# Kernel tuning notes

Hardware: AMD Instinct MI355X
Metric: run time of the kernel (lower is better)

The kernel has to match this reference:

```python
import jax, jax.numpy as jnp
import numpy as np

DIM = 512
QK_DIM = 128
HIDDEN = 1024


def setup_inputs() -> dict:
    key = jax.random.key(0)
    ks = jax.random.split(key, 8)
    b, n = 4, 4096
    x = jax.random.normal(ks[0], (b, n, DIM), dtype=jnp.float32)
    # nn.Linear(dim, hidden*2)
    w_hidden = jax.random.normal(ks[1], (DIM, 2 * HIDDEN), dtype=jnp.float32) / np.sqrt(DIM)
    b_hidden = jnp.zeros((2 * HIDDEN,), dtype=jnp.float32)
    # nn.Linear(dim, qk_dim, bias=False)
    w_qk = jax.random.normal(ks[2], (DIM, QK_DIM), dtype=jnp.float32) / np.sqrt(DIM)
    # OffsetScale params (gamma init 1, beta init 0; randomize slightly for a nontrivial test)
    q_gamma = 1.0 + 0.02 * jax.random.normal(ks[3], (QK_DIM,), dtype=jnp.float32)
    q_beta = 0.02 * jax.random.normal(ks[4], (QK_DIM,), dtype=jnp.float32)
    k_gamma = 1.0 + 0.02 * jax.random.normal(ks[5], (QK_DIM,), dtype=jnp.float32)
    k_beta = 0.02 * jax.random.normal(ks[6], (QK_DIM,), dtype=jnp.float32)
    # nn.Linear(hidden, dim)
    w_out = jax.random.normal(ks[7], (HIDDEN, DIM), dtype=jnp.float32) / np.sqrt(HIDDEN)
    b_out = jnp.zeros((DIM,), dtype=jnp.float32)
    return {
        "x": x,
        "w_hidden": w_hidden, "b_hidden": b_hidden,
        "w_qk": w_qk,
        "q_gamma": q_gamma, "q_beta": q_beta,
        "k_gamma": k_gamma, "k_beta": k_beta,
        "w_out": w_out, "b_out": b_out,
    }


def reference(x, w_hidden, b_hidden, w_qk, q_gamma, q_beta, k_gamma, k_beta, w_out, b_out):
    scale = QK_DIM ** -0.5
    # to_hidden -> chunk into v, gate (NOTE: source applies no activation here)
    hid = jnp.einsum('bnd,dh->bnh', x, w_hidden) + b_hidden  # [b, n, 2*hidden]
    v, gate = jnp.split(hid, 2, axis=-1)                     # each [b, n, hidden]
    qk = jnp.einsum('bnd,de->bne', x, w_qk)                  # [b, n, qk_dim]
    q = qk * q_gamma + q_beta
    k = qk * k_gamma + k_beta
    sim = jnp.einsum('bid,bjd->bij', q, k) * scale           # [b, n, n]
    attn = jnp.square(jax.nn.relu(sim))                      # ReLU^2, no softmax
    out = jnp.einsum('bij,bjh->bih', attn, v)                # [b, n, hidden]
    out = out * gate
    out = jnp.einsum('bnh,hd->bnd', out, w_out) + b_out      # [b, n, dim]
    return out + x  # add_residual=True
```

## Files before the change

### kernel.cpp

```cpp
#include <hip/hip_runtime.h>
#include <hip/hip_bf16.h>

typedef __attribute__((ext_vector_type(8))) short bf16x8;
typedef __attribute__((ext_vector_type(4))) float f32x4;
typedef unsigned short u16;

__device__ __forceinline__ u16 f2b(float f) {
  __hip_bfloat16 h = __float2bfloat16(f);
  return __builtin_bit_cast(unsigned short, h);
}
__device__ __forceinline__ float b2f(u16 u) {
  __hip_bfloat16 h = __builtin_bit_cast(__hip_bfloat16, u);
  return __bfloat162float(h);
}

#define BAR() __builtin_amdgcn_s_barrier()
#define LGKM0() do { asm volatile("s_waitcnt lgkmcnt(0)" ::: "memory"); __builtin_amdgcn_sched_barrier(0); } while (0)
#define LGKM4() do { asm volatile("s_waitcnt lgkmcnt(4)" ::: "memory"); __builtin_amdgcn_sched_barrier(0); } while (0)
#define LGKM8() do { asm volatile("s_waitcnt lgkmcnt(8)" ::: "memory"); __builtin_amdgcn_sched_barrier(0); } while (0)
#define VMCNT4() asm volatile("s_waitcnt vmcnt(4)" ::: "memory")
#define VMCNT0() asm volatile("s_waitcnt vmcnt(0)" ::: "memory")

#define EPI_HID 0
#define EPI_QK 1
#define EPI_ATTN 2
#define EPI_PV 3
#define EPI_OUT 4

__device__ __forceinline__ void stage_tile(char* sbase, const char* gbase, int ld_bytes, int tid) {
#pragma unroll
  for (int i = 0; i < 4; ++i) {
    int o = (i * 256 + tid) * 16;
    int row = o >> 7;
    int cb = o & 127;
    int scb = cb ^ ((row & 7) << 4);
    const char* src = gbase + (long)row * ld_bytes + scb;
    __builtin_amdgcn_global_load_lds((const __attribute__((address_space(1))) void*)src,
                                     (__attribute__((address_space(3))) void*)(sbase + o),
                                     16, 0, 0);
  }
}

template <int EPI>
__global__ __launch_bounds__(256, 2) void gemm_tn(
    const char* Ab, const char* Bb, long sAbat, long sBbat,
    int lda_b, int ldb_b, int nkt,
    u16* o0, u16* o1,
    const float* a0, const float* a1, const float* a2, const float* a3,
    float* fout, const float* xres) {
  __shared__ __align__(16) char lds[32768];
  char* sA = lds;
  char* sB = lds + 16384;
  const int tid = threadIdx.x;
  const int lane = tid & 63;
  const int wave = tid >> 6;
  const int wm = wave >> 1, wn = wave & 1;
  const int l16 = lane & 15, lq = lane >> 4;
  const int bat = blockIdx.z;
  const int row0 = blockIdx.y * 128;
  const int col0 = blockIdx.x * 128;

  const char* Abase = Ab + (long)bat * sAbat + (long)row0 * lda_b;
  const char* Bbase = Bb + (long)bat * sBbat + (long)col0 * ldb_b;

  f32x4 acc[4][4];
#pragma unroll
  for (int i = 0; i < 4; ++i)
#pragma unroll
    for (int j = 0; j < 4; ++j) acc[i][j] = (f32x4){0.f, 0.f, 0.f, 0.f};

  for (int kt = 0; kt < nkt; ++kt) {
    stage_tile(sA, Abase + (long)kt * 128, lda_b, tid);
    stage_tile(sB, Bbase + (long)kt * 128, ldb_b, tid);
    __syncthreads();
#pragma unroll
    for (int kk = 0; kk < 2; ++kk) {
      bf16x8 af[4], bfr[4];
#pragma unroll
      for (int mf = 0; mf < 4; ++mf) {
        int r = wm * 64 + mf * 16 + l16;
        int kb = kk * 64 + lq * 16;
        af[mf] = *(const bf16x8*)(sA + r * 128 + (kb ^ ((r & 7) << 4)));
      }
#pragma unroll
      for (int nf = 0; nf < 4; ++nf) {
        int r = wn * 64 + nf * 16 + l16;
        int kb = kk * 64 + lq * 16;
        bfr[nf] = *(const bf16x8*)(sB + r * 128 + (kb ^ ((r & 7) << 4)));
      }
#pragma unroll
      for (int mf = 0; mf < 4; ++mf)
#pragma unroll
        for (int nf = 0; nf < 4; ++nf)
          acc[mf][nf] = __builtin_amdgcn_mfma_f32_16x16x32_bf16(af[mf], bfr[nf], acc[mf][nf], 0, 0, 0);
    }
    __syncthreads();
  }

#pragma unroll
  for (int mf = 0; mf < 4; ++mf) {
#pragma unroll
    for (int nf = 0; nf < 4; ++nf) {
      const int row = row0 + wm * 64 + mf * 16 + lq * 4;
      const int col = col0 + wn * 64 + nf * 16 + l16;
      f32x4 v = acc[mf][nf];
      if constexpr (EPI == EPI_QK) {
        float qg = a0[col], qbt = a1[col], kg = a2[col], kbt = a3[col];
#pragma unroll
        for (int i = 0; i < 4; ++i) {
          float t = v[i];
          o0[(size_t)(row + i) * 128 + col] = f2b(t * qg + qbt);
          o1[(size_t)(row + i) * 128 + col] = f2b(t * kg + kbt);
        }
      } else if constexpr (EPI == EPI_OUT) {
        float bias = a0[col];
#pragma unroll
        for (int i = 0; i < 4; ++i)
          fout[(size_t)(row + i) * 512 + col] = v[i] + bias + xres[(size_t)(row + i) * 512 + col];
      }
    }
  }
}

__device__ __forceinline__ void stage_half(char* sbase, const char* gbase, long ld, int tid) {
#pragma unroll
  for (int i = 0; i < 2; ++i) {
    int o = (i * 512 + tid) * 16;
    int row = o >> 7;
    int cb = o & 127;
    int scb = cb ^ ((row & 7) << 4);
    const char* src = gbase + (long)row * ld + scb;
    __builtin_amdgcn_global_load_lds((const __attribute__((address_space(1))) void*)src,
                                     (__attribute__((address_space(3))) void*)(sbase + o),
                                     16, 0, 0);
  }
}

template <int EPI>
__global__ __launch_bounds__(512, 2) void gemm256(
    const char* Ab, const char* Bb, long sAbat, long sBbat,
    long lda, long ldb, int nkt, int nx,
    u16* o0, u16* o1,
    const float* a0, float* fout, const float* xres) {
  extern __shared__ __align__(16) char lds[];
  const int tid = threadIdx.x;
  const int lane = tid & 63;
  const int wave = tid >> 6;
  const int wm = wave >> 2;
  const int wn = wave & 3;
  const int l16 = lane & 15, lq = lane >> 4;
  const int bat = blockIdx.y;

  const int nwg = gridDim.x;
  const int qq = nwg >> 3;
  const int fid = blockIdx.x;
  const int swz = (fid & 7) * qq + (fid >> 3);
  const int row0 = (swz / nx) * 256;
  const int col0 = (swz % nx) * 256;

  const char* gA = Ab + (long)bat * sAbat + (long)row0 * lda;
  const char* gB = Bb + (long)bat * sBbat + (long)col0 * ldb;

  f32x4 acc[8][4];
#pragma unroll
  for (int i = 0; i < 8; ++i)
#pragma unroll
    for (int j = 0; j < 4; ++j) acc[i][j] = (f32x4){0.f, 0.f, 0.f, 0.f};

  const int kmask = (l16 & 7) << 4;
  const int kb0 = (lq * 16) ^ kmask;
  const int kb1 = (64 + lq * 16) ^ kmask;

  stage_half(lds + 32768, gB, ldb, tid);
  stage_half(lds + 32768 + 16384, gB + 128 * ldb, ldb, tid);
  stage_half(lds, gA, lda, tid);
  stage_half(lds + 16384, gA + 128 * lda, lda, tid);
  if (nkt > 1) {
    stage_half(lds + 65536 + 32768, gB + 128, ldb, tid);
    stage_half(lds + 65536 + 32768 + 16384, gB + 128 * ldb + 128, ldb, tid);
    VMCNT4();
  } else {
    VMCNT0();
  }
  BAR();

  bf16x8 af0[4], af1[4], afp0[4], afp1[4], bfr0[4], bfr1[4];

  for (int t = 0; t < nkt; ++t) {
    const char* buf = lds + (t & 1) * 65536;
    const char* myA = buf + wm * 16384;
    const char* myB = buf + 32768 + (wn >> 1) * 16384;
    const int rB = (wn & 1) * 64;
    char* stA = lds + ((t + 1) & 1) * 65536;
    char* stB = lds + (t & 1) * 65536 + 32768;
    const bool sA_ok = (t + 1) < nkt;
    const bool sB_ok = (t + 2) < nkt;

#pragma unroll
    for (int nf = 0; nf < 4; ++nf)
      bfr0[nf] = *(const bf16x8*)(myB + (rB + nf * 16 + l16) * 128 + kb0);
#pragma unroll
    for (int mf = 0; mf < 4; ++mf)
      af0[mf] = *(const bf16x8*)(myA + (mf * 16 + l16) * 128 + kb0);
#pragma unroll
    for (int nf = 0; nf < 4; ++nf)
      bfr1[nf] = *(const bf16x8*)(myB + (rB + nf * 16 + l16) * 128 + kb1);
#pragma unroll
    for (int mf = 0; mf < 4; ++mf)
      af1[mf] = *(const bf16x8*)(myA + (mf * 16 + l16) * 128 + kb1);
    if (sA_ok) stage_half(stA, gA + (long)(t + 1) * 128, lda, tid);
    BAR();
    LGKM8();
    __builtin_amdgcn_s_setprio(1);
#pragma unroll
    for (int mf = 0; mf < 4; ++mf)
#pragma unroll
      for (int nf = 0; nf < 4; ++nf)
        acc[mf][nf] = __builtin_amdgcn_mfma_f32_16x16x32_bf16(af0[mf], bfr0[nf], acc[mf][nf], 0, 0, 0);
    __builtin_amdgcn_s_setprio(0);
    BAR();

#pragma unroll
    for (int mf = 0; mf < 4; ++mf)
      afp0[mf] = *(const bf16x8*)(myA + (64 + mf * 16 + l16) * 128 + kb0);
    if (sA_ok) stage_half(stA + 16384, gA + 128 * lda + (long)(t + 1) * 128, lda, tid);
    BAR();
    LGKM4();
    __builtin_amdgcn_s_setprio(1);
#pragma unroll
    for (int mf = 0; mf < 4; ++mf)
#pragma unroll
      for (int nf = 0; nf < 4; ++nf)
        acc[mf][nf] = __builtin_amdgcn_mfma_f32_16x16x32_bf16(af1[mf], bfr1[nf], acc[mf][nf], 0, 0, 0);
    __builtin_amdgcn_s_setprio(0);
    BAR();

#pragma unroll
    for (int mf = 0; mf < 4; ++mf)
      afp1[mf] = *(const bf16x8*)(myA + (64 + mf * 16 + l16) * 128 + kb1);
    if (sB_ok) stage_half(stB, gB + (long)(t + 2) * 128, ldb, tid);
    BAR();
    LGKM4();
    __builtin_amdgcn_s_setprio(1);
#pragma unroll
    for (int mf = 0; mf < 4; ++mf)
#pragma unroll
      for (int nf = 0; nf < 4; ++nf)
        acc[4 + mf][nf] = __builtin_amdgcn_mfma_f32_16x16x32_bf16(afp0[mf], bfr0[nf], acc[4 + mf][nf], 0, 0, 0);
    __builtin_amdgcn_s_setprio(0);
    BAR();

    if (sB_ok) stage_half(stB + 16384, gB + 128 * ldb + (long)(t + 2) * 128, ldb, tid);
    BAR();
    LGKM0();
    __builtin_amdgcn_s_setprio(1);
#pragma unroll
    for (int mf = 0; mf < 4; ++mf)
#pragma unroll
      for (int nf = 0; nf < 4; ++nf)
        acc[4 + mf][nf] = __builtin_amdgcn_mfma_f32_16x16x32_bf16(afp1[mf], bfr1[nf], acc[4 + mf][nf], 0, 0, 0);
    __builtin_amdgcn_s_setprio(0);
    if (sB_ok) { VMCNT4(); } else if (sA_ok) { VMCNT0(); }
    BAR();
  }

#pragma unroll
  for (int mi = 0; mi < 8; ++mi) {
#pragma unroll
    for (int ni = 0; ni < 4; ++ni) {
      const int row = row0 + wm * 128 + mi * 16 + lq * 4;
      const int col = col0 + wn * 64 + ni * 16 + l16;
      f32x4 v = acc[mi][ni];
      if constexpr (EPI == EPI_HID) {
        float bias = a0[col];
        u16* dst = (col < 1024) ? (o0 + (size_t)col * 16384 + row)
                                : (o1 + (size_t)(col - 1024) * 16384 + row);
        *(ushort4*)dst = make_ushort4(f2b(v.x + bias), f2b(v.y + bias), f2b(v.z + bias), f2b(v.w + bias));
      } else if constexpr (EPI == EPI_ATTN) {
        const float scale = 0.088388347648318447f;
        u16* dst = o0 + (size_t)bat * 4096 * 4096;
#pragma unroll
        for (int i = 0; i < 4; ++i) {
          float t = v[i] * scale;
          t = t > 0.f ? t * t : 0.f;
          dst[(size_t)(row + i) * 4096 + col] = f2b(t);
        }
      } else if constexpr (EPI == EPI_PV) {
        const u16* gt = o1 + (size_t)col * 16384 + (size_t)bat * 4096 + row;
        ushort4 g = *(const ushort4*)gt;
        u16* dst = o0 + (size_t)bat * 4096 * 1024;
        dst[(size_t)(row + 0) * 1024 + col] = f2b(v.x * b2f(g.x));
        dst[(size_t)(row + 1) * 1024 + col] = f2b(v.y * b2f(g.y));
        dst[(size_t)(row + 2) * 1024 + col] = f2b(v.z * b2f(g.z));
        dst[(size_t)(row + 3) * 1024 + col] = f2b(v.w * b2f(g.w));
      }
    }
  }
}

__global__ void conv_b(const float* in, u16* out, int n) {
  int i = (blockIdx.x * blockDim.x + threadIdx.x) * 4;
  if (i >= n) return;
  float4 f = *(const float4*)(in + i);
  *(ushort4*)(out + i) = make_ushort4(f2b(f.x), f2b(f.y), f2b(f.z), f2b(f.w));
}

__global__ void transpose_b(const float* in, u16* out, int R, int C) {
  int o = blockIdx.x * blockDim.x + threadIdx.x;
  if (o >= R * C) return;
  int c = o / R, r = o - c * R;
  out[o] = f2b(in[(size_t)r * C + c]);
}

extern "C" void kernel_launch(void* const* d_in, const int* in_sizes, int n_in,
                              void* d_out, int out_size, void* d_ws, size_t ws_size,
                              hipStream_t stream) {
  const float* x = (const float*)d_in[0];
  const float* w_hidden = (const float*)d_in[1];
  const float* b_hidden = (const float*)d_in[2];
  const float* w_qk = (const float*)d_in[3];
  const float* q_gamma = (const float*)d_in[4];
  const float* q_beta = (const float*)d_in[5];
  const float* k_gamma = (const float*)d_in[6];
  const float* k_beta = (const float*)d_in[7];
  const float* w_out = (const float*)d_in[8];
  const float* b_out = (const float*)d_in[9];
  float* out = (float*)d_out;

  char* ws = (char*)d_ws;
  size_t off = 0;
  auto alloc = [&](size_t bytes) { char* p = ws + off; off += (bytes + 255) & ~255ull; return p; };
  u16* xb     = (u16*)alloc(16384ull * 512 * 2);
  u16* wh_t   = (u16*)alloc(2048ull * 512 * 2);
  u16* wqk_t  = (u16*)alloc(128ull * 512 * 2);
  u16* wout_t = (u16*)alloc(512ull * 1024 * 2);
  u16* v_t    = (u16*)alloc(1024ull * 16384 * 2);
  u16* g_t    = (u16*)alloc(1024ull * 16384 * 2);
  u16* qb_a   = (u16*)alloc(16384ull * 128 * 2);
  u16* kb_a   = (u16*)alloc(16384ull * 128 * 2);
  u16* attnb  = (u16*)alloc(4ull * 4096 * 4096 * 2);
  u16* out1b  = (u16*)alloc(16384ull * 1024 * 2);

  (void)hipFuncSetAttribute((const void*)gemm256<EPI_HID>, hipFuncAttributeMaxDynamicSharedMemorySize, 131072);
  (void)hipFuncSetAttribute((const void*)gemm256<EPI_ATTN>, hipFuncAttributeMaxDynamicSharedMemorySize, 131072);
  (void)hipFuncSetAttribute((const void*)gemm256<EPI_PV>, hipFuncAttributeMaxDynamicSharedMemorySize, 131072);

  conv_b<<<(16384 * 512 / 4 + 255) / 256, 256, 0, stream>>>(x, xb, 16384 * 512);
  transpose_b<<<(512 * 2048 + 255) / 256, 256, 0, stream>>>(w_hidden, wh_t, 512, 2048);
  transpose_b<<<(512 * 128 + 255) / 256, 256, 0, stream>>>(w_qk, wqk_t, 512, 128);
  transpose_b<<<(1024 * 512 + 255) / 256, 256, 0, stream>>>(w_out, wout_t, 1024, 512);

  gemm256<EPI_HID><<<dim3(512, 1), 512, 131072, stream>>>(
      (const char*)xb, (const char*)wh_t, 0, 0, 1024, 1024, 8, 8,
      v_t, g_t, b_hidden, nullptr, nullptr);
  gemm_tn<EPI_QK><<<dim3(1, 128, 1), 256, 0, stream>>>(
      (const char*)xb, (const char*)wqk_t, 0, 0, 1024, 1024, 8,
      qb_a, kb_a, q_gamma, q_beta, k_gamma, k_beta, nullptr, nullptr);
  gemm256<EPI_ATTN><<<dim3(256, 4), 512, 131072, stream>>>(
      (const char*)qb_a, (const char*)kb_a, 4096ll * 256, 4096ll * 256, 256, 256, 2, 16,
      attnb, nullptr, nullptr, nullptr, nullptr);
  gemm256<EPI_PV><<<dim3(64, 4), 512, 131072, stream>>>(
      (const char*)attnb, (const char*)v_t, 4096ll * 8192, 8192, 8192, 32768, 64, 4,
      out1b, g_t, nullptr, nullptr, nullptr);
  gemm_tn<EPI_OUT><<<dim3(4, 128, 1), 256, 0, stream>>>(
      (const char*)out1b, (const char*)wout_t, 0, 0, 2048, 2048, 16,
      nullptr, nullptr, b_out, nullptr, nullptr, nullptr, out, x);
}
```

Before: 322.8 us.

## Software-pipeline LDS fragment loads across k-tiles and route output GEMM through gemm256

The main 256x256 GEMM loop now prefetches the first-half A/B fragments for the next k-tile during the last MFMA phase. It also drops most of the per-phase workgroup barriers, keeping only one vmcnt-gated barrier before the next-tile reads plus one at loop end. Separately, the final output projection moves from the smaller gemm_tn kernel to gemm256 with the residual/bias epilogue, launched as 128 workgroups. Fewer barriers means less synchronisation stall, but removing them risks LDS races where staging overwrites buffers other waves may still be reading. The 128-block output launch may also underfill the GPU.

```diff
diff --git a/kernel.cpp b/kernel.cpp
--- a/kernel.cpp
+++ b/kernel.cpp
@@ -19,6 +19,7 @@
 #define LGKM4() do { asm volatile("s_waitcnt lgkmcnt(4)" ::: "memory"); __builtin_amdgcn_sched_barrier(0); } while (0)
 #define LGKM8() do { asm volatile("s_waitcnt lgkmcnt(8)" ::: "memory"); __builtin_amdgcn_sched_barrier(0); } while (0)
 #define VMCNT4() asm volatile("s_waitcnt vmcnt(4)" ::: "memory")
+#define VMCNT2() asm volatile("s_waitcnt vmcnt(2)" ::: "memory")
 #define VMCNT0() asm volatile("s_waitcnt vmcnt(0)" ::: "memory")
 
 #define EPI_HID 0
@@ -112,11 +113,6 @@
           o0[(size_t)(row + i) * 128 + col] = f2b(t * qg + qbt);
           o1[(size_t)(row + i) * 128 + col] = f2b(t * kg + kbt);
         }
-      } else if constexpr (EPI == EPI_OUT) {
-        float bias = a0[col];
-#pragma unroll
-        for (int i = 0; i < 4; ++i)
-          fout[(size_t)(row + i) * 512 + col] = v[i] + bias + xres[(size_t)(row + i) * 512 + col];
       }
     }
   }
@@ -170,6 +166,7 @@
   const int kmask = (l16 & 7) << 4;
   const int kb0 = (lq * 16) ^ kmask;
   const int kb1 = (64 + lq * 16) ^ kmask;
+  const int rB = (wn & 1) * 64;
 
   stage_half(lds + 32768, gB, ldb, tid);
   stage_half(lds + 32768 + 16384, gB + 128 * ldb, ldb, tid);
@@ -185,31 +182,36 @@
   BAR();
 
   bf16x8 af0[4], af1[4], afp0[4], afp1[4], bfr0[4], bfr1[4];
+  {
+    const char* myA = lds + wm * 16384;
+    const char* myB = lds + 32768 + (wn >> 1) * 16384;
+#pragma unroll
+    for (int nf = 0; nf < 4; ++nf)
+      bfr0[nf] = *(const bf16x8*)(myB + (rB + nf * 16 + l16) * 128 + kb0);
+#pragma unroll
+    for (int mf = 0; mf < 4; ++mf)
+      af0[mf] = *(const bf16x8*)(myA + (mf * 16 + l16) * 128 + kb0);
+  }
 
   for (int t = 0; t < nkt; ++t) {
-    const char* buf = lds + (t & 1) * 65536;
-    const char* myA = buf + wm * 16384;
-    const char* myB = buf + 32768 + (wn >> 1) * 16384;
-    const int rB = (wn & 1) * 64;
-    char* stA = lds + ((t + 1) & 1) * 65536;
-    char* stB = lds + (t & 1) * 65536 + 32768;
+    const char* bufc = lds + (t & 1) * 65536;
+    const char* bufn = lds + ((t + 1) & 1) * 65536;
+    const char* myA = bufc + wm * 16384;
+    const char* myB = bufc + 32768 + (wn >> 1) * 16384;
+    const char* nA = bufn + wm * 16384;
+    const char* nB = bufn + 32768 + (wn >> 1) * 16384;
+    char* stA = (char*)bufn;
+    char* stB = (char*)bufc + 32768;
     const bool sA_ok = (t + 1) < nkt;
     const bool sB_ok = (t + 2) < nkt;
 
 #pragma unroll
     for (int nf = 0; nf < 4; ++nf)
-      bfr0[nf] = *(const bf16x8*)(myB + (rB + nf * 16 + l16) * 128 + kb0);
-#pragma unroll
-    for (int mf = 0; mf < 4; ++mf)
-      af0[mf] = *(const bf16x8*)(myA + (mf * 16 + l16) * 128 + kb0);
-#pragma unroll
-    for (int nf = 0; nf < 4; ++nf)
       bfr1[nf] = *(const bf16x8*)(myB + (rB + nf * 16 + l16) * 128 + kb1);
 #pragma unroll
     for (int mf = 0; mf < 4; ++mf)
       af1[mf] = *(const bf16x8*)(myA + (mf * 16 + l16) * 128 + kb1);
     if (sA_ok) stage_half(stA, gA + (long)(t + 1) * 128, lda, tid);
-    BAR();
     LGKM8();
     __builtin_amdgcn_s_setprio(1);
 #pragma unroll
@@ -218,13 +220,11 @@
       for (int nf = 0; nf < 4; ++nf)
         acc[mf][nf] = __builtin_amdgcn_mfma_f32_16x16x32_bf16(af0[mf], bfr0[nf], acc[mf][nf], 0, 0, 0);
     __builtin_amdgcn_s_setprio(0);
-    BAR();
 
 #pragma unroll
     for (int mf = 0; mf < 4; ++mf)
       afp0[mf] = *(const bf16x8*)(myA + (64 + mf * 16 + l16) * 128 + kb0);
     if (sA_ok) stage_half(stA + 16384, gA + 128 * lda + (long)(t + 1) * 128, lda, tid);
-    BAR();
     LGKM4();
     __builtin_amdgcn_s_setprio(1);
 #pragma unroll
@@ -239,7 +239,6 @@
     for (int mf = 0; mf < 4; ++mf)
       afp1[mf] = *(const bf16x8*)(myA + (64 + mf * 16 + l16) * 128 + kb1);
     if (sB_ok) stage_half(stB, gB + (long)(t + 2) * 128, ldb, tid);
-    BAR();
     LGKM4();
     __builtin_amdgcn_s_setprio(1);
 #pragma unroll
@@ -248,11 +247,21 @@
       for (int nf = 0; nf < 4; ++nf)
         acc[4 + mf][nf] = __builtin_amdgcn_mfma_f32_16x16x32_bf16(afp0[mf], bfr0[nf], acc[4 + mf][nf], 0, 0, 0);
     __builtin_amdgcn_s_setprio(0);
-    BAR();
-
+    if (sA_ok) {
+      if (sB_ok) { VMCNT2(); } else { VMCNT0(); }
+      BAR();
+    }
+
+    if (sA_ok) {
+#pragma unroll
+      for (int nf = 0; nf < 4; ++nf)
+        bfr0[nf] = *(const bf16x8*)(nB + (rB + nf * 16 + l16) * 128 + kb0);
+#pragma unroll
+      for (int mf = 0; mf < 4; ++mf)
+        af0[mf] = *(const bf16x8*)(nA + (mf * 16 + l16) * 128 + kb0);
+    }
     if (sB_ok) stage_half(stB + 16384, gB + 128 * ldb + (long)(t + 2) * 128, ldb, tid);
-    BAR();
-    LGKM0();
+    if (sA_ok) { LGKM8(); } else { LGKM0(); }
     __builtin_amdgcn_s_setprio(1);
 #pragma unroll
     for (int mf = 0; mf < 4; ++mf)
@@ -260,7 +269,6 @@
       for (int nf = 0; nf < 4; ++nf)
         acc[4 + mf][nf] = __builtin_amdgcn_mfma_f32_16x16x32_bf16(afp1[mf], bfr1[nf], acc[4 + mf][nf], 0, 0, 0);
     __builtin_amdgcn_s_setprio(0);
-    if (sB_ok) { VMCNT4(); } else if (sA_ok) { VMCNT0(); }
     BAR();
   }
 
@@ -293,6 +301,11 @@
         dst[(size_t)(row + 1) * 1024 + col] = f2b(v.y * b2f(g.y));
         dst[(size_t)(row + 2) * 1024 + col] = f2b(v.z * b2f(g.z));
         dst[(size_t)(row + 3) * 1024 + col] = f2b(v.w * b2f(g.w));
+      } else if constexpr (EPI == EPI_OUT) {
+        float bias = a0[col];
+#pragma unroll
+        for (int i = 0; i < 4; ++i)
+          fout[(size_t)(row + i) * 512 + col] = v[i] + bias + xres[(size_t)(row + i) * 512 + col];
       }
     }
   }
@@ -344,6 +357,7 @@
   (void)hipFuncSetAttribute((const void*)gemm256<EPI_HID>, hipFuncAttributeMaxDynamicSharedMemorySize, 131072);
   (void)hipFuncSetAttribute((const void*)gemm256<EPI_ATTN>, hipFuncAttributeMaxDynamicSharedMemorySize, 131072);
   (void)hipFuncSetAttribute((const void*)gemm256<EPI_PV>, hipFuncAttributeMaxDynamicSharedMemorySize, 131072);
+  (void)hipFuncSetAttribute((const void*)gemm256<EPI_OUT>, hipFuncAttributeMaxDynamicSharedMemorySize, 131072);
 
   conv_b<<<(16384 * 512 / 4 + 255) / 256, 256, 0, stream>>>(x, xb, 16384 * 512);
   transpose_b<<<(512 * 2048 + 255) / 256, 256, 0, stream>>>(w_hidden, wh_t, 512, 2048);
@@ -362,7 +376,7 @@
   gemm256<EPI_PV><<<dim3(64, 4), 512, 131072, stream>>>(
       (const char*)attnb, (const char*)v_t, 4096ll * 8192, 8192, 8192, 32768, 64, 4,
       out1b, g_t, nullptr, nullptr, nullptr);
-  gemm_tn<EPI_OUT><<<dim3(4, 128, 1), 256, 0, stream>>>(
-      (const char*)out1b, (const char*)wout_t, 0, 0, 2048, 2048, 16,
-      nullptr, nullptr, b_out, nullptr, nullptr, nullptr, out, x);
-}
+  gemm256<EPI_OUT><<<dim3(128, 1), 512, 131072, stream>>>(
+      (const char*)out1b, (const char*)wout_t, 0, 0, 2048, 2048, 16, 2,
+      nullptr, nullptr, b_out, out, x);
+}
```

Result: slower. 343.7 us (+6.5%).
